# Kernel tuning notes

Measured on AMD Instinct MI355X. Metric: run time of the kernel, lower is better.

## Reference

```python
import jax, jax.numpy as jnp
import numpy as np

N_NODES = 50000
N_EDGES = 800000
NODE_DIM = 256
HIDDEN_DIM = 256
LN_EPS = 1e-5


def setup_inputs() -> dict:
    key = jax.random.key(0)
    ks = jax.random.split(key, 8)
    d, h = NODE_DIM, HIDDEN_DIM
    return {
        "node_features": jax.random.normal(ks[0], (N_NODES, d), jnp.float32),
        "src": jax.random.randint(ks[1], (N_EDGES,), 0, N_NODES, jnp.int32),
        "dst": jax.random.randint(ks[2], (N_EDGES,), 0, N_NODES, jnp.int32),
        "edge_weight": jax.random.uniform(ks[3], (N_EDGES,), jnp.float32),
        "W1": jax.random.normal(ks[4], (d, h), jnp.float32) / np.sqrt(d),
        "b1": jnp.zeros((h,), jnp.float32),
        "g1": jnp.ones((h,), jnp.float32),
        "be1": jnp.zeros((h,), jnp.float32),
        "W2": jax.random.normal(ks[5], (h, h), jnp.float32) / np.sqrt(h),
        "b2": jnp.zeros((h,), jnp.float32),
        "g2": jnp.ones((h,), jnp.float32),
        "be2": jnp.zeros((h,), jnp.float32),
        "Wp": jax.random.normal(ks[6], (h, d), jnp.float32) / np.sqrt(h),
        "bp": jnp.zeros((d,), jnp.float32),
    }


def _spmm(src, dst, w, x, n):
    # sparse adj @ x : agg[i] = sum_{edges e with dst=i} w_e * x[src_e]
    return jax.ops.segment_sum(w[:, None] * x[src], dst, num_segments=n)


def _layer_norm(x, g, b):
    mu = jnp.mean(x, -1, keepdims=True)
    var = jnp.mean(jnp.square(x - mu), -1, keepdims=True)
    return (x - mu) * jax.lax.rsqrt(var + LN_EPS) * g + b


def reference(node_features, src, dst, edge_weight, W1, b1, g1, be1, W2, b2, g2, be2, Wp, bp):
    n = node_features.shape[0]
    x = node_features
    for (W, b, g, be) in ((W1, b1, g1, be1), (W2, b2, g2, be2)):
        agg = _spmm(src, dst, edge_weight, x, n)
        h = (x + agg) @ W + b
        x = jax.nn.gelu(_layer_norm(h, g, be), approximate=False)
        # Dropout(0.1) is identity in eval mode
    return x @ Wp + bp
```

## Files before the change

kernel.cpp:

```cpp
#include <hip/hip_runtime.h>
#include <hip/hip_bf16.h>
#include <math.h>

#define N_NODES 50000
#define N_EDGES 800000
#define DIM 256
#define MPAD 50176
#define LN_EPS 1e-5f
#define SCAN_BLOCKS 196

typedef short bf16x8 __attribute__((ext_vector_type(8)));
typedef float f32x16 __attribute__((ext_vector_type(16)));
typedef unsigned short u16;
typedef u16 u16x8 __attribute__((ext_vector_type(8)));

__device__ __forceinline__ u16 f2bf(float f) {
    union { float f; unsigned u; } v; v.f = f;
    unsigned r = (v.u + 0x7FFFu + ((v.u >> 16) & 1u)) >> 16;
    return (u16)r;
}
__device__ __forceinline__ float bf2f(u16 h) {
    union { unsigned u; float f; } v; v.u = ((unsigned)h) << 16;
    return v.f;
}
__device__ __forceinline__ float gelu_f(float x) {
    float z = x * (1.595769122f + 0.0713548162726f * x * x);
    return x * (1.0f / (1.0f + __expf(-z)));
}

__global__ void count_kernel(const int* __restrict__ dst, int* __restrict__ counts) {
    int e = blockIdx.x * 256 + threadIdx.x;
    if (e < N_EDGES) atomicAdd(&counts[dst[e]], 1);
}

__global__ void scan1_kernel(const int* __restrict__ counts, int* __restrict__ offsets,
                             int* __restrict__ bsum) {
    __shared__ int sh[256];
    int t = threadIdx.x;
    int idx = blockIdx.x * 256 + t;
    int v = (idx < N_NODES) ? counts[idx] : 0;
    sh[t] = v;
    __syncthreads();
#pragma unroll
    for (int off = 1; off < 256; off <<= 1) {
        int u = (t >= off) ? sh[t - off] : 0;
        __syncthreads();
        sh[t] += u;
        __syncthreads();
    }
    if (idx < N_NODES) offsets[idx] = sh[t] - v;
    if (t == 255) bsum[blockIdx.x] = sh[255];
}

__global__ void scan2_kernel(const int* __restrict__ bsum, int* __restrict__ bbase) {
    __shared__ int sh[256];
    int t = threadIdx.x;
    int v = (t < SCAN_BLOCKS) ? bsum[t] : 0;
    sh[t] = v;
    __syncthreads();
#pragma unroll
    for (int off = 1; off < 256; off <<= 1) {
        int u = (t >= off) ? sh[t - off] : 0;
        __syncthreads();
        sh[t] += u;
        __syncthreads();
    }
    if (t < SCAN_BLOCKS) bbase[t] = sh[t] - v;
}

__global__ void scan3_kernel(int* __restrict__ offsets, const int* __restrict__ bbase,
                             int* __restrict__ cursor) {
    int idx = blockIdx.x * 256 + threadIdx.x;
    if (idx < N_NODES) {
        int o = offsets[idx] + bbase[blockIdx.x];
        offsets[idx] = o;
        cursor[idx] = o;
    }
    if (idx == 0) offsets[N_NODES] = N_EDGES;
}

__global__ void scatter_kernel(const int* __restrict__ src, const int* __restrict__ dst,
                               const float* __restrict__ w, int* __restrict__ cursor,
                               int2* __restrict__ ep) {
    int e = blockIdx.x * 256 + threadIdx.x;
    if (e < N_EDGES) {
        int d = dst[e];
        int p = atomicAdd(&cursor[d], 1);
        int2 v; v.x = src[e]; v.y = __float_as_int(w[e]);
        ep[p] = v;
    }
}

__global__ void conv_kernel(const float* __restrict__ in, u16* __restrict__ out) {
    int i = blockIdx.x * 256 + threadIdx.x;
    float4 v = ((const float4*)in)[i];
    ushort4 o;
    o.x = f2bf(v.x); o.y = f2bf(v.y); o.z = f2bf(v.z); o.w = f2bf(v.w);
    ((ushort4*)out)[i] = o;
}

__global__ void convw_kernel(const float* __restrict__ W1, const float* __restrict__ W2,
                             const float* __restrict__ Wp, u16* __restrict__ WT) {
    int idx = blockIdx.x * 256 + threadIdx.x;
    int m = idx >> 16;
    int r = idx & 65535;
    int n = r >> 8, k = r & 255;
    const float* W = (m == 0) ? W1 : (m == 1) ? W2 : Wp;
    WT[idx] = f2bf(W[k * 256 + n]);
}

__global__ __launch_bounds__(256) void spmm_kernel(
        const u16* __restrict__ x, const int* __restrict__ offs,
        const int2* __restrict__ ep, u16* __restrict__ y) {
    int tid = threadIdx.x;
    int wave = tid >> 6;
    int lane = tid & 63;
    int l31 = lane & 31, half = lane >> 5;
    int node0 = blockIdx.x * 16 + wave * 4;

    const u16x8* xv = (const u16x8*)x;
#pragma unroll 1
    for (int i = 0; i < 4; ++i) {
        int node = node0 + i;
        float acc[8];
#pragma unroll
        for (int j = 0; j < 8; ++j) acc[j] = 0.f;
        if (node < N_NODES) {
            if (half == 0) {
                u16x8 sv = xv[(size_t)node * 32 + l31];
#pragma unroll
                for (int j = 0; j < 8; ++j) acc[j] = bf2f(sv[j]);
            }
            int p = offs[node];
            int p1 = offs[node + 1];
            for (; p + 4 <= p1; p += 4) {
                int2 e0 = ep[p + half];
                int2 e1 = ep[p + 2 + half];
                int s0 = e0.x; float w0 = __int_as_float(e0.y);
                int s1 = e1.x; float w1 = __int_as_float(e1.y);
                u16x8 v0 = xv[(size_t)s0 * 32 + l31];
                u16x8 v1 = xv[(size_t)s1 * 32 + l31];
#pragma unroll
                for (int j = 0; j < 8; ++j) acc[j] += w0 * bf2f(v0[j]);
#pragma unroll
                for (int j = 0; j < 8; ++j) acc[j] += w1 * bf2f(v1[j]);
            }
            if (p + 2 <= p1) {
                int2 e0 = ep[p + half];
                int s0 = e0.x; float w0 = __int_as_float(e0.y);
                u16x8 v0 = xv[(size_t)s0 * 32 + l31];
#pragma unroll
                for (int j = 0; j < 8; ++j) acc[j] += w0 * bf2f(v0[j]);
                p += 2;
            }
            if (p < p1) {
                int2 e0 = ep[p];
                int s0 = e0.x;
                float w0 = half ? 0.f : __int_as_float(e0.y);
                u16x8 v0 = xv[(size_t)s0 * 32 + l31];
#pragma unroll
                for (int j = 0; j < 8; ++j) acc[j] += w0 * bf2f(v0[j]);
            }
        }
#pragma unroll
        for (int j = 0; j < 8; ++j) acc[j] += __shfl_xor(acc[j], 32);
        if (half == 0) {
            u16x8 o;
#pragma unroll
            for (int j = 0; j < 8; ++j) o[j] = f2bf(acc[j]);
            int tile = node >> 5, m = node & 31;
            int gi = (l31 >> 1) * 64 + (l31 & 1) * 32 + m;
            *(u16x8*)(y + (size_t)tile * 8192 + (size_t)gi * 8) = o;
        }
    }
}

template <int MODE, int OUT_TILED>
__global__ __launch_bounds__(256, 1) void gemm_kernel(
        const u16* __restrict__ A, const u16* __restrict__ BT,
        const float* __restrict__ bias, const float* __restrict__ g,
        const float* __restrict__ be, u16* __restrict__ xb_out,
        float* __restrict__ f_out) {
    __shared__ u16 b_lds[128 * 520];
    int tid = threadIdx.x;
    int wave = tid >> 6, lane = tid & 63;
    int l31 = lane & 31, half = lane >> 5;

#pragma unroll 8
    for (int i = 0; i < 32; ++i) {
        int s = i * 256 + tid;
        u16x8 v = *(const u16x8*)(BT + (size_t)s * 8);
        int n = s >> 5, kc = s & 31;
        int t = n >> 5, n32 = n & 31, kb = kc >> 1, hf = kc & 1;
        *(u16x8*)&b_lds[(t * 16 + kb) * 520 + hf * 256 + n32 * 8] = v;
    }

    int tile0 = blockIdx.x * 8 + wave * 2;
    const u16* ga0 = A + (size_t)tile0 * 8192 + lane * 8;
    const u16* ga1 = ga0 + 8192;
    bf16x8 p0 = *(const bf16x8*)ga0;
    bf16x8 p1 = *(const bf16x8*)ga1;

    f32x16 acc[2][8];
#pragma unroll
    for (int rf = 0; rf < 2; ++rf)
#pragma unroll
        for (int t = 0; t < 8; ++t)
#pragma unroll
            for (int r = 0; r < 16; ++r) acc[rf][t][r] = 0.f;

    __syncthreads();

#pragma unroll
    for (int kb = 0; kb < 16; ++kb) {
        bf16x8 a0 = p0, a1 = p1;
        if (kb < 15) {
            p0 = *(const bf16x8*)(ga0 + (kb + 1) * 512);
            p1 = *(const bf16x8*)(ga1 + (kb + 1) * 512);
        }
        const u16* bl = &b_lds[kb * 520 + lane * 8];
#pragma unroll
        for (int t = 0; t < 8; ++t) {
            bf16x8 bf = *(const bf16x8*)(bl + t * 16 * 520);
            acc[0][t] = __builtin_amdgcn_mfma_f32_32x32x16_bf16(a0, bf, acc[0][t], 0, 0, 0);
            acc[1][t] = __builtin_amdgcn_mfma_f32_32x32x16_bf16(a1, bf, acc[1][t], 0, 0, 0);
        }
    }

    float bv[8];
#pragma unroll
    for (int t = 0; t < 8; ++t) bv[t] = bias[t * 32 + l31];

#pragma unroll
    for (int rf = 0; rf < 2; ++rf) {
        int tile = tile0 + rf;
        if (MODE == 0) {
            float gv[8], bev[8];
#pragma unroll
            for (int t = 0; t < 8; ++t) {
                int c = t * 32 + l31;
                gv[t] = g[c]; bev[t] = be[c];
            }
#pragma unroll
            for (int r = 0; r < 16; ++r) {
                float s = 0.f, q = 0.f;
#pragma unroll
                for (int t = 0; t < 8; ++t) {
                    float v = acc[rf][t][r] + bv[t];
                    acc[rf][t][r] = v;
                    s += v; q += v * v;
                }
                for (int off = 1; off < 32; off <<= 1) {
                    s += __shfl_xor(s, off);
                    q += __shfl_xor(q, off);
                }
                float mu = s * (1.0f / 256.0f);
                float var = q * (1.0f / 256.0f) - mu * mu;
                float rs = rsqrtf(var + LN_EPS);
                int m = (r & 3) + 8 * (r >> 2) + 4 * half;
                int row = tile * 32 + m;
#pragma unroll
                for (int t = 0; t < 8; ++t) {
                    int c = t * 32 + l31;
                    float v = (acc[rf][t][r] - mu) * rs * gv[t] + bev[t];
                    u16 ob = f2bf(gelu_f(v));
                    if (OUT_TILED) {
                        size_t o = (size_t)tile * 8192 +
                                   ((size_t)(c >> 4) * 64 + ((c >> 3) & 1) * 32 + m) * 8 + (c & 7);
                        xb_out[o] = ob;
                    } else {
                        xb_out[(size_t)row * 256 + c] = ob;
                    }
                }
            }
        } else {
#pragma unroll
            for (int r = 0; r < 16; ++r) {
                int m = (r & 3) + 8 * (r >> 2) + 4 * half;
                int row = tile * 32 + m;
                if (row < N_NODES) {
#pragma unroll
                    for (int t = 0; t < 8; ++t) {
                        int c = t * 32 + l31;
                        f_out[(size_t)row * 256 + c] = acc[rf][t][r] + bv[t];
                    }
                }
            }
        }
    }
}

extern "C" void kernel_launch(void* const* d_in, const int* in_sizes, int n_in,
                              void* d_out, int out_size, void* d_ws, size_t ws_size,
                              hipStream_t stream) {
    const float* nodef = (const float*)d_in[0];
    const int*   src   = (const int*)d_in[1];
    const int*   dst   = (const int*)d_in[2];
    const float* ew    = (const float*)d_in[3];
    const float* W1 = (const float*)d_in[4];
    const float* b1 = (const float*)d_in[5];
    const float* g1 = (const float*)d_in[6];
    const float* be1 = (const float*)d_in[7];
    const float* W2 = (const float*)d_in[8];
    const float* b2 = (const float*)d_in[9];
    const float* g2 = (const float*)d_in[10];
    const float* be2 = (const float*)d_in[11];
    const float* Wp = (const float*)d_in[12];
    const float* bp = (const float*)d_in[13];
    float* out = (float*)d_out;

    char* ws = (char*)d_ws;
    size_t off = 0;
    auto alloc = [&](size_t bytes) -> void* {
        void* p = ws + off;
        off += (bytes + 255) & ~(size_t)255;
        return p;
    };
    u16*   ybuf    = (u16*)alloc((size_t)MPAD * 256 * 2);
    u16*   xbuf    = (u16*)alloc((size_t)MPAD * 256 * 2);
    u16*   WT      = (u16*)alloc((size_t)3 * 65536 * 2);
    int*   counts  = (int*)alloc((size_t)N_NODES * 4);
    int*   offsets = (int*)alloc((size_t)(N_NODES + 1) * 4);
    int*   cursor  = (int*)alloc((size_t)N_NODES * 4);
    int2*  ep      = (int2*)alloc((size_t)N_EDGES * 8);
    int*   bsum    = (int*)alloc((size_t)SCAN_BLOCKS * 4);
    int*   bbase   = (int*)alloc((size_t)SCAN_BLOCKS * 4);

    hipMemsetAsync(counts, 0, (size_t)N_NODES * 4, stream);
    count_kernel<<<(N_EDGES + 255) / 256, 256, 0, stream>>>(dst, counts);
    scan1_kernel<<<SCAN_BLOCKS, 256, 0, stream>>>(counts, offsets, bsum);
    scan2_kernel<<<1, 256, 0, stream>>>(bsum, bbase);
    scan3_kernel<<<SCAN_BLOCKS, 256, 0, stream>>>(offsets, bbase, cursor);
    scatter_kernel<<<(N_EDGES + 255) / 256, 256, 0, stream>>>(src, dst, ew, cursor, ep);
    conv_kernel<<<N_NODES * 64 / 256, 256, 0, stream>>>(nodef, xbuf);
    convw_kernel<<<768, 256, 0, stream>>>(W1, W2, Wp, WT);

    const int GB = MPAD / 256;
    const int SB = MPAD / 16;
    spmm_kernel<<<SB, 256, 0, stream>>>(xbuf, offsets, ep, ybuf);
    gemm_kernel<0, 0><<<GB, 256, 0, stream>>>(ybuf, WT, b1, g1, be1, xbuf, nullptr);
    spmm_kernel<<<SB, 256, 0, stream>>>(xbuf, offsets, ep, ybuf);
    gemm_kernel<0, 1><<<GB, 256, 0, stream>>>(ybuf, WT + 65536, b2, g2, be2, ybuf, nullptr);
    gemm_kernel<1, 0><<<GB, 256, 0, stream>>>(ybuf, WT + 2 * 65536, bp, nullptr, nullptr, nullptr, out);
}
```

Measured before the change: 478.3 us.

## Pad CSR rows to multiples of eight and stage SpMM output through LDS

Each node's edge list is rounded up to a multiple of 8 entries, and the padding is zero-filled, so the SpMM inner loop becomes branch-free. It issues 16-byte edge loads and four gathers per iteration per half-wave, with no tail cases. Each block now handles 32 nodes and stages results in shared memory, then writes the tiled output layout as fully coalesced contiguous 16-byte stores. The cost is a larger edge buffer with an extra memset, and padded entries that still gather row 0 with weight zero, about 40% more gather work on average.

```diff
diff --git a/kernel.cpp b/kernel.cpp
--- a/kernel.cpp
+++ b/kernel.cpp
@@ -4,6 +4,7 @@
 
 #define N_NODES 50000
 #define N_EDGES 800000
+#define EP_PAD  1150000
 #define DIM 256
 #define MPAD 50176
 #define LN_EPS 1e-5f
@@ -38,7 +39,7 @@
     __shared__ int sh[256];
     int t = threadIdx.x;
     int idx = blockIdx.x * 256 + t;
-    int v = (idx < N_NODES) ? counts[idx] : 0;
+    int v = (idx < N_NODES) ? ((counts[idx] + 7) & ~7) : 0;
     sh[t] = v;
     __syncthreads();
 #pragma unroll
@@ -69,14 +70,14 @@
 }
 
 __global__ void scan3_kernel(int* __restrict__ offsets, const int* __restrict__ bbase,
-                             int* __restrict__ cursor) {
+                             const int* __restrict__ counts, int* __restrict__ cursor) {
     int idx = blockIdx.x * 256 + threadIdx.x;
     if (idx < N_NODES) {
         int o = offsets[idx] + bbase[blockIdx.x];
         offsets[idx] = o;
         cursor[idx] = o;
-    }
-    if (idx == 0) offsets[N_NODES] = N_EDGES;
+        if (idx == N_NODES - 1) offsets[N_NODES] = o + ((counts[idx] + 7) & ~7);
+    }
 }
 
 __global__ void scatter_kernel(const int* __restrict__ src, const int* __restrict__ dst,
@@ -112,15 +113,16 @@
 __global__ __launch_bounds__(256) void spmm_kernel(
         const u16* __restrict__ x, const int* __restrict__ offs,
         const int2* __restrict__ ep, u16* __restrict__ y) {
+    __shared__ u16 tile[32 * 264];
     int tid = threadIdx.x;
     int wave = tid >> 6;
     int lane = tid & 63;
     int l31 = lane & 31, half = lane >> 5;
-    int node0 = blockIdx.x * 16 + wave * 4;
+    int node0 = blockIdx.x * 32 + wave * 8;
 
     const u16x8* xv = (const u16x8*)x;
 #pragma unroll 1
-    for (int i = 0; i < 4; ++i) {
+    for (int i = 0; i < 8; ++i) {
         int node = node0 + i;
         float acc[8];
 #pragma unroll
@@ -131,35 +133,27 @@
 #pragma unroll
                 for (int j = 0; j < 8; ++j) acc[j] = bf2f(sv[j]);
             }
-            int p = offs[node];
+            int p  = offs[node] + half * 2;
             int p1 = offs[node + 1];
-            for (; p + 4 <= p1; p += 4) {
-                int2 e0 = ep[p + half];
-                int2 e1 = ep[p + 2 + half];
-                int s0 = e0.x; float w0 = __int_as_float(e0.y);
-                int s1 = e1.x; float w1 = __int_as_float(e1.y);
+            for (; p < p1; p += 8) {
+                int4 ea = *(const int4*)&ep[p];
+                int4 eb = *(const int4*)&ep[p + 4];
+                int s0 = ea.x; float w0 = __int_as_float(ea.y);
+                int s1 = ea.z; float w1 = __int_as_float(ea.w);
+                int s2 = eb.x; float w2 = __int_as_float(eb.y);
+                int s3 = eb.z; float w3 = __int_as_float(eb.w);
                 u16x8 v0 = xv[(size_t)s0 * 32 + l31];
                 u16x8 v1 = xv[(size_t)s1 * 32 + l31];
+                u16x8 v2 = xv[(size_t)s2 * 32 + l31];
+                u16x8 v3 = xv[(size_t)s3 * 32 + l31];
 #pragma unroll
                 for (int j = 0; j < 8; ++j) acc[j] += w0 * bf2f(v0[j]);
 #pragma unroll
                 for (int j = 0; j < 8; ++j) acc[j] += w1 * bf2f(v1[j]);
-            }
-            if (p + 2 <= p1) {
-                int2 e0 = ep[p + half];
-                int s0 = e0.x; float w0 = __int_as_float(e0.y);
-                u16x8 v0 = xv[(size_t)s0 * 32 + l31];
-#pragma unroll
-                for (int j = 0; j < 8; ++j) acc[j] += w0 * bf2f(v0[j]);
-                p += 2;
-            }
-            if (p < p1) {
-                int2 e0 = ep[p];
-                int s0 = e0.x;
-                float w0 = half ? 0.f : __int_as_float(e0.y);
-                u16x8 v0 = xv[(size_t)s0 * 32 + l31];
-#pragma unroll
-                for (int j = 0; j < 8; ++j) acc[j] += w0 * bf2f(v0[j]);
+#pragma unroll
+                for (int j = 0; j < 8; ++j) acc[j] += w2 * bf2f(v2[j]);
+#pragma unroll
+                for (int j = 0; j < 8; ++j) acc[j] += w3 * bf2f(v3[j]);
             }
         }
 #pragma unroll
@@ -168,10 +162,19 @@
             u16x8 o;
 #pragma unroll
             for (int j = 0; j < 8; ++j) o[j] = f2bf(acc[j]);
-            int tile = node >> 5, m = node & 31;
-            int gi = (l31 >> 1) * 64 + (l31 & 1) * 32 + m;
-            *(u16x8*)(y + (size_t)tile * 8192 + (size_t)gi * 8) = o;
-        }
+            *(u16x8*)&tile[(wave * 8 + i) * 264 + l31 * 8] = o;
+        }
+    }
+    __syncthreads();
+    u16* outb = y + (size_t)blockIdx.x * 8192;
+#pragma unroll
+    for (int hh = 0; hh < 4; ++hh) {
+        int gi = tid + hh * 256;
+        int kb = gi >> 6;
+        int rem = gi & 63;
+        int hf = rem >> 5, m = rem & 31;
+        u16x8 v = *(const u16x8*)&tile[m * 264 + kb * 16 + hf * 8];
+        *(u16x8*)(outb + (size_t)gi * 8) = v;
     }
 }
 
@@ -322,21 +325,22 @@
     int*   counts  = (int*)alloc((size_t)N_NODES * 4);
     int*   offsets = (int*)alloc((size_t)(N_NODES + 1) * 4);
     int*   cursor  = (int*)alloc((size_t)N_NODES * 4);
-    int2*  ep      = (int2*)alloc((size_t)N_EDGES * 8);
+    int2*  ep      = (int2*)alloc((size_t)EP_PAD * 8);
     int*   bsum    = (int*)alloc((size_t)SCAN_BLOCKS * 4);
     int*   bbase   = (int*)alloc((size_t)SCAN_BLOCKS * 4);
 
     hipMemsetAsync(counts, 0, (size_t)N_NODES * 4, stream);
+    hipMemsetAsync(ep, 0, (size_t)EP_PAD * 8, stream);
     count_kernel<<<(N_EDGES + 255) / 256, 256, 0, stream>>>(dst, counts);
     scan1_kernel<<<SCAN_BLOCKS, 256, 0, stream>>>(counts, offsets, bsum);
     scan2_kernel<<<1, 256, 0, stream>>>(bsum, bbase);
-    scan3_kernel<<<SCAN_BLOCKS, 256, 0, stream>>>(offsets, bbase, cursor);
+    scan3_kernel<<<SCAN_BLOCKS, 256, 0, stream>>>(offsets, bbase, counts, cursor);
     scatter_kernel<<<(N_EDGES + 255) / 256, 256, 0, stream>>>(src, dst, ew, cursor, ep);
     conv_kernel<<<N_NODES * 64 / 256, 256, 0, stream>>>(nodef, xbuf);
     convw_kernel<<<768, 256, 0, stream>>>(W1, W2, Wp, WT);
 
     const int GB = MPAD / 256;
-    const int SB = MPAD / 16;
+    const int SB = MPAD / 32;
     spmm_kernel<<<SB, 256, 0, stream>>>(xbuf, offsets, ep, ybuf);
     gemm_kernel<0, 0><<<GB, 256, 0, stream>>>(ybuf, WT, b1, g1, be1, xbuf, nullptr);
     spmm_kernel<<<SB, 256, 0, stream>>>(xbuf, offsets, ep, ybuf);
```

After: 624.1 us. 1.3x slower.
